# Kernel tuning notes

Measured on AMD Instinct MI355X. Metric: run time of the kernel, lower is better.

Reference implementation:

```python
import jax, jax.numpy as jnp
import numpy as np

NUM_HEADS = 8

def setup_inputs() -> dict:
    key = jax.random.key(0)
    ks = jax.random.split(key, 5)
    B, T, N, D = 2, 8, 1024, 512
    x = jax.random.normal(ks[0], (B, T, N, D), dtype=jnp.float32)
    s = 1.0 / np.sqrt(D)
    W_qkv = jax.random.normal(ks[1], (D, 3 * D), dtype=jnp.float32) * s
    b_qkv = jnp.zeros((3 * D,), dtype=jnp.float32)
    W_proj = jax.random.normal(ks[2], (D, D), dtype=jnp.float32) * s
    b_proj = jnp.zeros((D,), dtype=jnp.float32)
    return {"x": x, "W_qkv": W_qkv, "b_qkv": b_qkv, "W_proj": W_proj, "b_proj": b_proj}

def reference(x, W_qkv, b_qkv, W_proj, b_proj):
    B, T, N, D = x.shape
    H = NUM_HEADS
    hd = D // H
    scale = hd ** -0.5
    xf = x.reshape(B * T, N, D)  # fold frames into batch
    qkv = xf @ W_qkv + b_qkv  # (BT, N, 3D)
    qkv = qkv.reshape(B * T, N, 3, H, hd)
    q = qkv[:, :, 0].transpose(0, 2, 1, 3)  # (BT, H, N, hd)
    k = qkv[:, :, 1].transpose(0, 2, 1, 3)
    v = qkv[:, :, 2].transpose(0, 2, 1, 3)
    attn = jnp.einsum('bhnd,bhmd->bhnm', q, k) * scale
    attn = jax.nn.softmax(attn, axis=-1)  # dropout is identity in eval mode
    out = jnp.einsum('bhnm,bhmd->bhnd', attn, v)
    out = out.transpose(0, 2, 1, 3).reshape(B * T, N, D)
    out = out @ W_proj + b_proj
    return out.reshape(B, T, N, D)
```

## Files before the change

### kernel.cpp

```cpp
#include <hip/hip_runtime.h>

typedef __bf16 b16x8 __attribute__((ext_vector_type(8)));
typedef float f32x4 __attribute__((ext_vector_type(4)));
typedef float f32x16 __attribute__((ext_vector_type(16)));
typedef unsigned int u32;

static __device__ __forceinline__ f32x4 mfma16(b16x8 a, b16x8 b, f32x4 c) {
  return __builtin_amdgcn_mfma_f32_16x16x32_bf16(a, b, c, 0, 0, 0);
}
static __device__ __forceinline__ f32x16 mfma32(b16x8 a, b16x8 b, f32x16 c) {
  return __builtin_amdgcn_mfma_f32_32x32x16_bf16(a, b, c, 0, 0, 0);
}

static __device__ __forceinline__ unsigned short f2bf(float f) {
  unsigned u = __builtin_bit_cast(unsigned, f);
  u += 0x7fffu + ((u >> 16) & 1u);
  return (unsigned short)(u >> 16);
}
static __device__ __forceinline__ u32 cvtpk(float lo, float hi) {
  u32 d;
  asm("v_cvt_pk_bf16_f32 %0, %1, %2" : "=v"(d) : "v"(lo), "v"(hi));
  return d;
}
static __device__ __forceinline__ float ex2(float x) {
#if __has_builtin(__builtin_amdgcn_exp2f)
  return __builtin_amdgcn_exp2f(x);
#else
  return exp2f(x);
#endif
}

static __device__ __forceinline__ void gload16(const void* g, void* s) {
  __builtin_amdgcn_global_load_lds((const __attribute__((address_space(1))) void*)g,
                                   (__attribute__((address_space(3))) void*)s, 16, 0, 0);
}

__global__ __launch_bounds__(256) void cvt_x(const float* __restrict__ in,
                                             unsigned short* __restrict__ out, int n8) {
  int i = blockIdx.x * 256 + threadIdx.x;
  if (i >= n8) return;
  const float4* p = (const float4*)in + (size_t)2 * i;
  float4 a = p[0], b = p[1];
  unsigned r0 = f2bf(a.x) | ((unsigned)f2bf(a.y) << 16);
  unsigned r1 = f2bf(a.z) | ((unsigned)f2bf(a.w) << 16);
  unsigned r2 = f2bf(b.x) | ((unsigned)f2bf(b.y) << 16);
  unsigned r3 = f2bf(b.z) | ((unsigned)f2bf(b.w) << 16);
  ((uint4*)out)[i] = make_uint4(r0, r1, r2, r3);
}

__global__ __launch_bounds__(256) void tr_w(const float* __restrict__ in,
                                            unsigned short* __restrict__ out, int R, int C) {
  int idx = blockIdx.x * 256 + threadIdx.x;
  if (idx >= R * C) return;
  int r = idx / C, c = idx % C;
  out[(size_t)c * R + r] = f2bf(in[idx]);
}

template <int MODE>
__global__ __launch_bounds__(256) void gemm_bt_bias(const unsigned short* __restrict__ A,
                                                    const unsigned short* __restrict__ Bt,
                                                    const float* __restrict__ bias,
                                                    void* __restrict__ Cout, int M, int N, int K) {
  __shared__ unsigned short As[128 * 64];
  __shared__ unsigned short Bs[128 * 64];
  const int tid = threadIdx.x;
  const int w = tid >> 6, l = tid & 63, g = l >> 4, lm = l & 15;
  const int wr = w >> 1, wc = w & 1;
  const int bm = blockIdx.y, bn = blockIdx.x;

  f32x4 acc[4][4];
#pragma unroll
  for (int i = 0; i < 4; ++i)
#pragma unroll
    for (int j = 0; j < 4; ++j) acc[i][j] = {0.f, 0.f, 0.f, 0.f};

  const int Kb = K * 2;
  const char* Abase = (const char*)A + (size_t)(bm * 128) * Kb;
  const char* Bbase = (const char*)Bt + (size_t)(bn * 128) * Kb;
  const int lrow = l >> 3;
  const int srccol = ((l & 7) * 16) ^ (((l >> 3) & 7) << 4);

  for (int kt = 0; kt < K; kt += 64) {
#pragma unroll
    for (int i = w; i < 16; i += 4) {
      gload16(Abase + (size_t)(i * 8 + lrow) * Kb + kt * 2 + srccol, As + i * 512);
      gload16(Bbase + (size_t)(i * 8 + lrow) * Kb + kt * 2 + srccol, Bs + i * 512);
    }
    __syncthreads();
#pragma unroll
    for (int ks = 0; ks < 2; ++ks) {
      b16x8 af[4], bf[4];
#pragma unroll
      for (int rt = 0; rt < 4; ++rt) {
        int row = wr * 64 + rt * 16 + lm;
        af[rt] = *(const b16x8*)((const char*)As + row * 128 +
                                 (((ks * 64) + g * 16) ^ ((lm & 7) << 4)));
      }
#pragma unroll
      for (int ct = 0; ct < 4; ++ct) {
        int row = wc * 64 + ct * 16 + lm;
        bf[ct] = *(const b16x8*)((const char*)Bs + row * 128 +
                                 (((ks * 64) + g * 16) ^ ((lm & 7) << 4)));
      }
#pragma unroll
      for (int rt = 0; rt < 4; ++rt)
#pragma unroll
        for (int ct = 0; ct < 4; ++ct) acc[rt][ct] = mfma16(af[rt], bf[ct], acc[rt][ct]);
    }
    __syncthreads();
  }

#pragma unroll
  for (int ct = 0; ct < 4; ++ct) {
    int col = bn * 128 + wc * 64 + ct * 16 + lm;
    float bv = bias[col];
    float sc = (MODE == 1 && col < 512) ? 0.18033688011112042f : 1.0f;
#pragma unroll
    for (int rt = 0; rt < 4; ++rt) {
      int row0 = bm * 128 + wr * 64 + rt * 16 + g * 4;
#pragma unroll
      for (int j = 0; j < 4; ++j) {
        float v = (acc[rt][ct][j] + bv) * sc;
        if (MODE == 2)
          ((float*)Cout)[(size_t)(row0 + j) * N + col] = v;
        else
          ((unsigned short*)Cout)[(size_t)(row0 + j) * N + col] = f2bf(v);
      }
    }
  }
}

__global__ __launch_bounds__(256) void attn_kernel(const unsigned short* __restrict__ qkv,
                                                   unsigned short* __restrict__ out) {
  __shared__ unsigned short Ks[64 * 64];
  __shared__ unsigned short Vt[64 * 72];
  __shared__ unsigned short Ps[4 * 32 * 72];

  const int tid = threadIdx.x;
  const int w = tid >> 6, l = tid & 63, g = l >> 4, lm = l & 15;
  const int lq = l & 31, hi = l >> 5;
  const int id = blockIdx.x;
  const int id2 = (id & 7) * 128 + (id >> 3);
  const int qt = id2 & 7, h = (id2 >> 3) & 7, bt = id2 >> 6;
  const size_t rb = (size_t)bt * 1024;

  const int qrow_sw = qt * 128 + w * 32 + lq;
  b16x8 qf[4];
#pragma unroll
  for (int ks = 0; ks < 4; ++ks)
    qf[ks] = *(const b16x8*)(qkv + (rb + qrow_sw) * 1536 + h * 64 + ks * 16 + hi * 8);

  f32x4 o[2][4];
#pragma unroll
  for (int rt = 0; rt < 2; ++rt)
#pragma unroll
    for (int dt = 0; dt < 4; ++dt) o[rt][dt] = {0.f, 0.f, 0.f, 0.f};
  float m = -1e30f, lsum = 0.f;

  const int krow_l = l >> 3;
  const int srccol = ((l & 7) * 16) ^ (((l >> 3) & 7) << 4);
  const char* kbase = (const char*)(qkv + rb * 1536 + 512 + (size_t)h * 64);
  const unsigned short* vbase = qkv + rb * 1536 + 1024 + (size_t)h * 64 + w * 16;
  unsigned short* Psw = Ps + w * 32 * 72;

  uint4 va = *(const uint4*)(vbase + (size_t)l * 1536);
  uint4 vb = *(const uint4*)(vbase + (size_t)l * 1536 + 8);

  for (int kb = 0; kb < 16; ++kb) {
    const int k0 = kb * 64;
#pragma unroll
    for (int ii = 0; ii < 2; ++ii) {
      int i = w * 2 + ii;
      gload16(kbase + (size_t)(k0 + i * 8 + krow_l) * 3072 + srccol, Ks + i * 512);
    }
    {
      u32 vv[8] = {va.x, va.y, va.z, va.w, vb.x, vb.y, vb.z, vb.w};
#pragma unroll
      for (int k2 = 0; k2 < 8; ++k2) {
        int d0 = w * 16 + 2 * k2;
        Vt[d0 * 72 + l] = (unsigned short)(vv[k2] & 0xffffu);
        Vt[(d0 + 1) * 72 + l] = (unsigned short)(vv[k2] >> 16);
      }
    }
    __syncthreads();

    {
      int kn = ((kb + 1) & 15) * 64;
      va = *(const uint4*)(vbase + (size_t)(kn + l) * 1536);
      vb = *(const uint4*)(vbase + (size_t)(kn + l) * 1536 + 8);
    }

    f32x16 s0 = {0.f, 0.f, 0.f, 0.f, 0.f, 0.f, 0.f, 0.f, 0.f, 0.f, 0.f, 0.f, 0.f, 0.f, 0.f, 0.f};
    f32x16 s1 = s0;
#pragma unroll
    for (int ks = 0; ks < 4; ++ks) {
      int co = (ks * 32 + hi * 16) ^ ((lq & 7) << 4);
      b16x8 k0f = *(const b16x8*)((const char*)Ks + lq * 128 + co);
      b16x8 k1f = *(const b16x8*)((const char*)Ks + (32 + lq) * 128 + co);
      s0 = mfma32(k0f, qf[ks], s0);
      s1 = mfma32(k1f, qf[ks], s1);
    }

    float mx = -1e30f;
#pragma unroll
    for (int r = 0; r < 16; ++r) mx = fmaxf(mx, fmaxf(s0[r], s1[r]));
    mx = fmaxf(mx, __shfl_xor(mx, 32));
    if (!__all(mx <= m + 11.5f)) {
      float mn = fmaxf(m, mx);
      float resc = ex2(m - mn);
      m = mn;
      lsum *= resc;
#pragma unroll
      for (int rt = 0; rt < 2; ++rt) {
        float r0 = __shfl(resc, rt * 16 + g * 4 + 0);
        float r1 = __shfl(resc, rt * 16 + g * 4 + 1);
        float r2 = __shfl(resc, rt * 16 + g * 4 + 2);
        float r3 = __shfl(resc, rt * 16 + g * 4 + 3);
#pragma unroll
        for (int dt = 0; dt < 4; ++dt) {
          o[rt][dt][0] *= r0;
          o[rt][dt][1] *= r1;
          o[rt][dt][2] *= r2;
          o[rt][dt][3] *= r3;
        }
      }
    }
#pragma unroll
    for (int r = 0; r < 16; ++r) {
      s0[r] = ex2(s0[r] - m);
      s1[r] = ex2(s1[r] - m);
    }
    float a0 = 0.f, a1 = 0.f, a2 = 0.f, a3 = 0.f;
#pragma unroll
    for (int r = 0; r < 16; r += 4) {
      a0 += s0[r]; a1 += s0[r + 1]; a2 += s0[r + 2]; a3 += s0[r + 3];
      a0 += s1[r]; a1 += s1[r + 1]; a2 += s1[r + 2]; a3 += s1[r + 3];
    }
    float rs = (a0 + a1) + (a2 + a3);
    rs += __shfl_xor(rs, 32);
    lsum += rs;

#pragma unroll
    for (int gi = 0; gi < 4; ++gi) {
      int kidx = 8 * gi + 4 * hi;
      *(uint2*)(Psw + lq * 72 + kidx) =
          make_uint2(cvtpk(s0[4 * gi], s0[4 * gi + 1]), cvtpk(s0[4 * gi + 2], s0[4 * gi + 3]));
      *(uint2*)(Psw + lq * 72 + 32 + kidx) =
          make_uint2(cvtpk(s1[4 * gi], s1[4 * gi + 1]), cvtpk(s1[4 * gi + 2], s1[4 * gi + 3]));
    }

#pragma unroll
    for (int ks = 0; ks < 2; ++ks) {
      b16x8 pa[2];
#pragma unroll
      for (int rt = 0; rt < 2; ++rt)
        pa[rt] = *(const b16x8*)(Psw + (rt * 16 + lm) * 72 + ks * 32 + g * 8);
#pragma unroll
      for (int dt = 0; dt < 4; ++dt) {
        b16x8 vf = *(const b16x8*)(Vt + (dt * 16 + lm) * 72 + ks * 32 + g * 8);
        o[0][dt] = mfma16(pa[0], vf, o[0][dt]);
        o[1][dt] = mfma16(pa[1], vf, o[1][dt]);
      }
    }
    __syncthreads();
  }

  float inv = 1.0f / lsum;
#pragma unroll
  for (int rt = 0; rt < 2; ++rt) {
    float i0 = __shfl(inv, rt * 16 + g * 4 + 0);
    float i1 = __shfl(inv, rt * 16 + g * 4 + 1);
    float i2 = __shfl(inv, rt * 16 + g * 4 + 2);
    float i3 = __shfl(inv, rt * 16 + g * 4 + 3);
    float iv[4] = {i0, i1, i2, i3};
#pragma unroll
    for (int dt = 0; dt < 4; ++dt)
#pragma unroll
      for (int j = 0; j < 4; ++j) {
        int nrow = qt * 128 + w * 32 + rt * 16 + g * 4 + j;
        out[(rb + nrow) * 512 + h * 64 + dt * 16 + lm] = f2bf(o[rt][dt][j] * iv[j]);
      }
  }
}

extern "C" void kernel_launch(void* const* d_in, const int* in_sizes, int n_in, void* d_out,
                              int out_size, void* d_ws, size_t ws_size, hipStream_t stream) {
  const float* x = (const float*)d_in[0];
  const float* Wqkv = (const float*)d_in[1];
  const float* bqkv = (const float*)d_in[2];
  const float* Wproj = (const float*)d_in[3];
  const float* bproj = (const float*)d_in[4];
  float* outp = (float*)d_out;

  char* ws = (char*)d_ws;
  unsigned short* xb = (unsigned short*)(ws);
  unsigned short* wqkvT = (unsigned short*)(ws + 16777216);
  unsigned short* wprojT = (unsigned short*)(ws + 18350080);
  unsigned short* qkvb = (unsigned short*)(ws + 18874368);
  unsigned short* attno = (unsigned short*)(ws + 69206016);

  cvt_x<<<4096, 256, 0, stream>>>(x, xb, 1048576);
  tr_w<<<3072, 256, 0, stream>>>(Wqkv, wqkvT, 512, 1536);
  tr_w<<<1024, 256, 0, stream>>>(Wproj, wprojT, 512, 512);
  gemm_bt_bias<1><<<dim3(12, 128), 256, 0, stream>>>(xb, wqkvT, bqkv, qkvb, 16384, 1536, 512);
  attn_kernel<<<1024, 256, 0, stream>>>(qkvb, attno);
  gemm_bt_bias<2><<<dim3(4, 128), 256, 0, stream>>>(attno, wprojT, bproj, outp, 16384, 512, 512);
}
```

Before: 233.3 us.

## Load K directly to registers, double-buffer V, remap GEMM blocks across XCDs, add setprio

```diff
diff --git a/kernel.cpp b/kernel.cpp
--- a/kernel.cpp
+++ b/kernel.cpp
@@ -60,13 +60,16 @@
 __global__ __launch_bounds__(256) void gemm_bt_bias(const unsigned short* __restrict__ A,
                                                     const unsigned short* __restrict__ Bt,
                                                     const float* __restrict__ bias,
-                                                    void* __restrict__ Cout, int M, int N, int K) {
+                                                    void* __restrict__ Cout, int M, int N, int K,
+                                                    int nbx) {
   __shared__ unsigned short As[128 * 64];
   __shared__ unsigned short Bs[128 * 64];
   const int tid = threadIdx.x;
   const int w = tid >> 6, l = tid & 63, g = l >> 4, lm = l & 15;
   const int wr = w >> 1, wc = w & 1;
-  const int bm = blockIdx.y, bn = blockIdx.x;
+  const int per = gridDim.x >> 3;
+  const int wg = (blockIdx.x & 7) * per + (blockIdx.x >> 3);
+  const int bm = wg / nbx, bn = wg % nbx;
 
   f32x4 acc[4][4];
 #pragma unroll
@@ -102,10 +105,12 @@
         bf[ct] = *(const b16x8*)((const char*)Bs + row * 128 +
                                  (((ks * 64) + g * 16) ^ ((lm & 7) << 4)));
       }
+      __builtin_amdgcn_s_setprio(1);
 #pragma unroll
       for (int rt = 0; rt < 4; ++rt)
 #pragma unroll
         for (int ct = 0; ct < 4; ++ct) acc[rt][ct] = mfma16(af[rt], bf[ct], acc[rt][ct]);
+      __builtin_amdgcn_s_setprio(0);
     }
     __syncthreads();
   }
@@ -132,8 +137,7 @@
 
 __global__ __launch_bounds__(256) void attn_kernel(const unsigned short* __restrict__ qkv,
                                                    unsigned short* __restrict__ out) {
-  __shared__ unsigned short Ks[64 * 64];
-  __shared__ unsigned short Vt[64 * 72];
+  __shared__ unsigned short Vt[2][64 * 72];
   __shared__ unsigned short Ps[4 * 32 * 72];
 
   const int tid = threadIdx.x;
@@ -157,48 +161,65 @@
     for (int dt = 0; dt < 4; ++dt) o[rt][dt] = {0.f, 0.f, 0.f, 0.f};
   float m = -1e30f, lsum = 0.f;
 
-  const int krow_l = l >> 3;
-  const int srccol = ((l & 7) * 16) ^ (((l >> 3) & 7) << 4);
-  const char* kbase = (const char*)(qkv + rb * 1536 + 512 + (size_t)h * 64);
+  const unsigned short* kbase = qkv + rb * 1536 + 512 + (size_t)h * 64 + hi * 8;
   const unsigned short* vbase = qkv + rb * 1536 + 1024 + (size_t)h * 64 + w * 16;
   unsigned short* Psw = Ps + w * 32 * 72;
 
   uint4 va = *(const uint4*)(vbase + (size_t)l * 1536);
   uint4 vb = *(const uint4*)(vbase + (size_t)l * 1536 + 8);
+  b16x8 kf0[4], kf1[4];
+#pragma unroll
+  for (int ks = 0; ks < 4; ++ks) {
+    kf0[ks] = *(const b16x8*)(kbase + (size_t)lq * 1536 + ks * 16);
+    kf1[ks] = *(const b16x8*)(kbase + (size_t)(32 + lq) * 1536 + ks * 16);
+  }
+  {
+    u32 vv[8] = {va.x, va.y, va.z, va.w, vb.x, vb.y, vb.z, vb.w};
+#pragma unroll
+    for (int k2 = 0; k2 < 8; ++k2) {
+      int d0 = w * 16 + 2 * k2;
+      Vt[0][d0 * 72 + l] = (unsigned short)(vv[k2] & 0xffffu);
+      Vt[0][(d0 + 1) * 72 + l] = (unsigned short)(vv[k2] >> 16);
+    }
+  }
+  va = *(const uint4*)(vbase + (size_t)(64 + l) * 1536);
+  vb = *(const uint4*)(vbase + (size_t)(64 + l) * 1536 + 8);
+  __syncthreads();
+  int cur = 0;
 
   for (int kb = 0; kb < 16; ++kb) {
-    const int k0 = kb * 64;
-#pragma unroll
-    for (int ii = 0; ii < 2; ++ii) {
-      int i = w * 2 + ii;
-      gload16(kbase + (size_t)(k0 + i * 8 + krow_l) * 3072 + srccol, Ks + i * 512);
+    f32x16 s0 = {0.f, 0.f, 0.f, 0.f, 0.f, 0.f, 0.f, 0.f, 0.f, 0.f, 0.f, 0.f, 0.f, 0.f, 0.f, 0.f};
+    f32x16 s1 = s0;
+    __builtin_amdgcn_s_setprio(1);
+#pragma unroll
+    for (int ks = 0; ks < 4; ++ks) {
+      s0 = mfma32(kf0[ks], qf[ks], s0);
+      s1 = mfma32(kf1[ks], qf[ks], s1);
+    }
+    __builtin_amdgcn_s_setprio(0);
+
+    {
+      int kn = ((kb + 1) & 15) * 64;
+#pragma unroll
+      for (int ks = 0; ks < 4; ++ks) {
+        kf0[ks] = *(const b16x8*)(kbase + (size_t)(kn + lq) * 1536 + ks * 16);
+        kf1[ks] = *(const b16x8*)(kbase + (size_t)(kn + 32 + lq) * 1536 + ks * 16);
+      }
     }
     {
       u32 vv[8] = {va.x, va.y, va.z, va.w, vb.x, vb.y, vb.z, vb.w};
+      unsigned short* Vn = Vt[cur ^ 1];
 #pragma unroll
       for (int k2 = 0; k2 < 8; ++k2) {
         int d0 = w * 16 + 2 * k2;
-        Vt[d0 * 72 + l] = (unsigned short)(vv[k2] & 0xffffu);
-        Vt[(d0 + 1) * 72 + l] = (unsigned short)(vv[k2] >> 16);
-      }
-    }
-    __syncthreads();
-
+        Vn[d0 * 72 + l] = (unsigned short)(vv[k2] & 0xffffu);
+        Vn[(d0 + 1) * 72 + l] = (unsigned short)(vv[k2] >> 16);
+      }
+    }
     {
-      int kn = ((kb + 1) & 15) * 64;
-      va = *(const uint4*)(vbase + (size_t)(kn + l) * 1536);
-      vb = *(const uint4*)(vbase + (size_t)(kn + l) * 1536 + 8);
-    }
-
-    f32x16 s0 = {0.f, 0.f, 0.f, 0.f, 0.f, 0.f, 0.f, 0.f, 0.f, 0.f, 0.f, 0.f, 0.f, 0.f, 0.f, 0.f};
-    f32x16 s1 = s0;
-#pragma unroll
-    for (int ks = 0; ks < 4; ++ks) {
-      int co = (ks * 32 + hi * 16) ^ ((lq & 7) << 4);
-      b16x8 k0f = *(const b16x8*)((const char*)Ks + lq * 128 + co);
-      b16x8 k1f = *(const b16x8*)((const char*)Ks + (32 + lq) * 128 + co);
-      s0 = mfma32(k0f, qf[ks], s0);
-      s1 = mfma32(k1f, qf[ks], s1);
+      int vn = ((kb + 2) & 15) * 64;
+      va = *(const uint4*)(vbase + (size_t)(vn + l) * 1536);
+      vb = *(const uint4*)(vbase + (size_t)(vn + l) * 1536 + 8);
     }
 
     float mx = -1e30f;
@@ -255,14 +276,17 @@
 #pragma unroll
       for (int rt = 0; rt < 2; ++rt)
         pa[rt] = *(const b16x8*)(Psw + (rt * 16 + lm) * 72 + ks * 32 + g * 8);
+      __builtin_amdgcn_s_setprio(1);
 #pragma unroll
       for (int dt = 0; dt < 4; ++dt) {
-        b16x8 vf = *(const b16x8*)(Vt + (dt * 16 + lm) * 72 + ks * 32 + g * 8);
+        b16x8 vf = *(const b16x8*)(&Vt[cur][0] + (dt * 16 + lm) * 72 + ks * 32 + g * 8);
         o[0][dt] = mfma16(pa[0], vf, o[0][dt]);
         o[1][dt] = mfma16(pa[1], vf, o[1][dt]);
       }
+      __builtin_amdgcn_s_setprio(0);
     }
     __syncthreads();
+    cur ^= 1;
   }
 
   float inv = 1.0f / lsum;
@@ -302,7 +326,7 @@
   cvt_x<<<4096, 256, 0, stream>>>(x, xb, 1048576);
   tr_w<<<3072, 256, 0, stream>>>(Wqkv, wqkvT, 512, 1536);
   tr_w<<<1024, 256, 0, stream>>>(Wproj, wprojT, 512, 512);
-  gemm_bt_bias<1><<<dim3(12, 128), 256, 0, stream>>>(xb, wqkvT, bqkv, qkvb, 16384, 1536, 512);
+  gemm_bt_bias<1><<<1536, 256, 0, stream>>>(xb, wqkvT, bqkv, qkvb, 16384, 1536, 512, 12);
   attn_kernel<<<1024, 256, 0, stream>>>(qkvb, attno);
-  gemm_bt_bias<2><<<dim3(4, 128), 256, 0, stream>>>(attno, wprojT, bproj, outp, 16384, 512, 512);
-}
+  gemm_bt_bias<2><<<512, 256, 0, stream>>>(attno, wprojT, bproj, outp, 16384, 512, 512, 4);
+}
```

Measured after the change: 239.9 us. 2.8% more time.
